# Kernel tuning notes

Measured on AMD Instinct MI355X. Metric: run time of the kernel, lower is better.

Reference implementation:

```python
import jax, jax.numpy as jnp
import numpy as np
from jax import lax

MAX_ITERATIONS = 20


def _min_pool3(x):
    # 3x3x3 min-pool, stride 1, padding 1. Equivalent to -max_pool3d(-x) in
    # torch: padded positions behave as +inf for the min (init value).
    return lax.reduce_window(
        x, jnp.inf, lax.min,
        window_dimensions=(1, 1, 3, 3, 3),
        window_strides=(1, 1, 1, 1, 1),
        padding=[(0, 0), (0, 0), (1, 1), (1, 1), (1, 1)])


def _accumulated_erosion(x, n_iters):
    # dist = sum_{k=1..n} erode^k(x). Torch's early-exit when curr.sum()==0 is
    # a no-op mathematically (erosion of all-zeros stays zero), so a fixed-
    # length scan computes the identical result.
    def body(carry, _):
        curr, dist = carry
        curr = _min_pool3(curr)
        return (curr, dist + curr), None
    (_, dist), _ = lax.scan(body, (x, jnp.zeros_like(x)), None, length=n_iters)
    return dist


def compute_fast_distance_map(target, max_iterations=MAX_ITERATIONS):
    # target: [B, 1, D, H, W] binary float
    dist_in = _accumulated_erosion(target, max_iterations)
    dist_out = _accumulated_erosion(1.0 - target, max_iterations)
    return dist_out * (1.0 - target) - (dist_in - 1.0) * target


def setup_inputs() -> dict:
    key = jax.random.key(0)
    k1, k2 = jax.random.split(key)
    inputs = jax.random.normal(k1, (4, 2, 96, 192, 192), dtype=jnp.float32)
    targets = jax.random.randint(k2, (4, 1, 96, 192, 192), 0, 2, dtype=jnp.int32)
    return {"inputs": inputs, "targets": targets}


def reference(inputs, targets):
    probs = jax.nn.softmax(inputs, axis=1)            # [B, C, D, H, W]
    t = targets.astype(jnp.float32)                   # [B, 1, D, H, W]
    no_fg = jnp.sum(t, axis=(2, 3, 4), keepdims=True) == 0
    dist_map_fg = compute_fast_distance_map(t, MAX_ITERATIONS)
    dist_map_fg = jnp.where(no_fg, jnp.ones_like(dist_map_fg), dist_map_fg)
    probs_fg = probs[:, 1]                            # [B, D, H, W]
    loss = jnp.mean(probs_fg * dist_map_fg[:, 0])
    return loss
```

## Files before the change

kernel.cpp:

```cpp
#include <hip/hip_runtime.h>
#include <hip/hip_bf16.h>

#define BATCH 4
#define DZ 96
#define DY 192
#define DX 192
#define ZS (DY * DX)
#define SVOL ((size_t)DZ * ZS)
#define NTOT ((double)(BATCH * (double)SVOL))
#define VOX_PER_THREAD 8
#define BLOCK 256
#define BLOCKS_PER_BATCH ((int)(SVOL / (VOX_PER_THREAD * BLOCK)))
#define GRID (BATCH * BLOCKS_PER_BATCH)

__device__ __noinline__ int far_dist(const int* __restrict__ T, size_t bOff,
                                     int z, int y, int x, int tv) {
    for (int r = 2; r <= 20; ++r) {
        int zlo = max(z - r, 0), zhi = min(z + r, DZ - 1);
        int ylo = max(y - r, 0), yhi = min(y + r, DY - 1);
        int xlo = max(x - r, 0), xhi = min(x + r, DX - 1);
        for (int zz = zlo; zz <= zhi; ++zz)
            for (int yy = ylo; yy <= yhi; ++yy) {
                const int* rp = T + bOff + (size_t)zz * ZS + (size_t)yy * DX;
                for (int xx = xlo; xx <= xhi; ++xx)
                    if (rp[xx] != tv) return r;
            }
    }
    return 21;
}

__global__ __launch_bounds__(BLOCK) void boundary_loss_kernel(
    const float* __restrict__ inp,
    const int* __restrict__ tgt,
    float4* __restrict__ P)
{
    const int b = blockIdx.x / BLOCKS_PER_BATCH;
    const size_t bOff = (size_t)b * SVOL;
    const int gid = blockIdx.x * BLOCK + threadIdx.x;
    const size_t vox = (size_t)gid * VOX_PER_THREAD;
    const int rem = (int)(vox - bOff);
    const int z = rem / ZS;
    const int ry = rem - z * ZS;
    const int y = ry / DX;
    const int x0 = ry - y * DX;

    uint32_t mxo = ~0u, mxa = 0u;
    if (x0 == 0)      { mxo &= ~1u;        mxa |= 1u; }
    if (x0 == DX - 8) { mxo &= ~(1u << 9); mxa |= (1u << 9); }
    const int ax = (x0 == 0) ? 0 : x0 - 4;
    const int dx8 = (x0 == DX - 8) ? DX - 1 : x0 + 8;

    uint32_t OR9 = 0u, AND9 = ~0u, pc = 0u;
    const int* Tb = tgt + bOff;
    #pragma unroll
    for (int dz = -1; dz <= 1; ++dz) {
        int zz = z + dz;
        if (zz < 0 || zz >= DZ) continue;
        #pragma unroll
        for (int dy = -1; dy <= 1; ++dy) {
            int yy = y + dy;
            if (yy < 0 || yy >= DY) continue;
            const int* rp = Tb + (size_t)zz * ZS + (size_t)yy * DX;
            int4 a = *(const int4*)(rp + ax);
            int4 q = *(const int4*)(rp + x0);
            int4 c = *(const int4*)(rp + x0 + 4);
            int  dd = rp[dx8];
            uint32_t p = (uint32_t)a.w
                | ((uint32_t)q.x << 1) | ((uint32_t)q.y << 2)
                | ((uint32_t)q.z << 3) | ((uint32_t)q.w << 4)
                | ((uint32_t)c.x << 5) | ((uint32_t)c.y << 6)
                | ((uint32_t)c.z << 7) | ((uint32_t)c.w << 8)
                | ((uint32_t)dd  << 9);
            if (dz == 0 && dy == 0) pc = p;
            uint32_t po = p & mxo;
            uint32_t pa = p | mxa;
            OR9  |= po | (po >> 1) | (po >> 2);
            AND9 &= pa & (pa >> 1) & (pa >> 2);
        }
    }
    const uint32_t diff8 = (OR9 ^ AND9) & 0xFFu;
    const uint32_t tc8   = (pc >> 1) & 0xFFu;

    const size_t sp = (size_t)z * ZS + (size_t)y * DX + x0;
    const float* i0 = inp + ((size_t)(2 * b)) * SVOL + sp;
    const float* i1 = i0 + SVOL;
    float4 A0 = *(const float4*)(i0), A1 = *(const float4*)(i0 + 4);
    float4 B0 = *(const float4*)(i1), B1 = *(const float4*)(i1 + 4);
    float c0[8] = {A0.x, A0.y, A0.z, A0.w, A1.x, A1.y, A1.z, A1.w};
    float c1[8] = {B0.x, B0.y, B0.z, B0.w, B1.x, B1.y, B1.z, B1.w};

    float s1 = 0.f, s2 = 0.f;
    #pragma unroll
    for (int i = 0; i < VOX_PER_THREAD; ++i) {
        float e   = __expf(c0[i] - c1[i]);
        float sig = __builtin_amdgcn_rcpf(1.0f + e);
        int ti = (int)((tc8 >> i) & 1u);
        float val = (float)ti;
        if (!((diff8 >> i) & 1u)) {
            int D = far_dist(tgt, bOff, z, y, x0 + i, ti);
            int mm = min(D - 1, 20);
            val = ti ? (1.0f - (float)mm) : (float)mm;
        }
        s1 = fmaf(sig, val, s1);
        s2 += sig;
    }
    float s3 = (tc8 != 0u) ? 1.f : 0.f;

    #pragma unroll
    for (int off = 32; off > 0; off >>= 1) {
        s1 += __shfl_down(s1, off);
        s2 += __shfl_down(s2, off);
        s3 += __shfl_down(s3, off);
    }
    __shared__ float red1[BLOCK / 64], red2[BLOCK / 64], red3[BLOCK / 64];
    const int lane = threadIdx.x & 63, wid = threadIdx.x >> 6;
    if (lane == 0) { red1[wid] = s1; red2[wid] = s2; red3[wid] = s3; }
    __syncthreads();
    if (threadIdx.x == 0) {
        P[blockIdx.x] = make_float4(red1[0] + red1[1] + red1[2] + red1[3],
                                    red2[0] + red2[1] + red2[2] + red2[3],
                                    red3[0] + red3[1] + red3[2] + red3[3], 0.f);
    }
}

__global__ __launch_bounds__(1024) void reduce_kernel(
    const float4* __restrict__ P, float* __restrict__ out)
{
    const int tid = threadIdx.x;
    const int lane = tid & 63, wid = tid >> 6;
    __shared__ double L1[16], L2[16], L3[16];
    double tot = 0.0;

    for (int b = 0; b < BATCH; ++b) {
        double d1 = 0.0, d2 = 0.0, d3 = 0.0;
        for (int i = tid; i < BLOCKS_PER_BATCH; i += 1024) {
            float4 p = P[b * BLOCKS_PER_BATCH + i];
            d1 += p.x; d2 += p.y; d3 += p.z;
        }
        #pragma unroll
        for (int off = 32; off > 0; off >>= 1) {
            d1 += __shfl_down(d1, off);
            d2 += __shfl_down(d2, off);
            d3 += __shfl_down(d3, off);
        }
        if (lane == 0) { L1[wid] = d1; L2[wid] = d2; L3[wid] = d3; }
        __syncthreads();
        if (tid == 0) {
            double s1 = 0.0, s2 = 0.0, s3 = 0.0;
            #pragma unroll
            for (int w = 0; w < 16; ++w) { s1 += L1[w]; s2 += L2[w]; s3 += L3[w]; }
            tot += (s3 > 0.0) ? s1 : s2;
        }
        __syncthreads();
    }
    if (tid == 0) out[0] = (float)(tot / NTOT);
}

extern "C" void kernel_launch(void* const* d_in, const int* in_sizes, int n_in,
                              void* d_out, int out_size, void* d_ws, size_t ws_size,
                              hipStream_t stream) {
    const float* inp = (const float*)d_in[0];
    const int*   tgt = (const int*)d_in[1];
    float* out = (float*)d_out;
    float4* P = (float4*)d_ws;

    hipLaunchKernelGGL(boundary_loss_kernel, dim3(GRID), dim3(BLOCK), 0, stream,
                       inp, tgt, P);
    hipLaunchKernelGGL(reduce_kernel, dim3(1), dim3(1024), 0, stream, P, out);
}
```

Measured before the change: 250.3 us.

## Tile target into LDS bitmask and reuse z-planes across a per-thread column

Each block now covers a 4x16 z-y tile of full x-rows. It packs the target halo into a shared-memory bitmask using atomicOr, and each thread walks 4 z-slices with 12 voxels per slice, reusing the 3x3 neighbourhood plane masks in a rolling window. This replaces the 9 redundant global int4 row loads per thread with LDS bit-window reads, cutting target-read traffic. Costs are LDS atomics, fewer blocks, a larger per-thread register footprint, and clamped halo handling that must still match the border semantics.

```diff
diff --git a/kernel.cpp b/kernel.cpp
--- a/kernel.cpp
+++ b/kernel.cpp
@@ -7,11 +7,20 @@
 #define DX 192
 #define ZS (DY * DX)
 #define SVOL ((size_t)DZ * ZS)
-#define NTOT ((double)(BATCH * (double)SVOL))
-#define VOX_PER_THREAD 8
+#define NTOT ((double)(4.0 * (double)SVOL))
+
+#define ZT 4
+#define YT 16
+#define NZT (DZ / ZT)
+#define NYT (DY / YT)
+#define BLOCKS_PER_BATCH (NZT * NYT)
+#define GRID (BATCH * BLOCKS_PER_BATCH)
 #define BLOCK 256
-#define BLOCKS_PER_BATCH ((int)(SVOL / (VOX_PER_THREAD * BLOCK)))
-#define GRID (BATCH * BLOCKS_PER_BATCH)
+
+#define NP (ZT + 2)
+#define NR (YT + 2)
+#define ROWW 8
+#define LDSW (NP * NR * ROWW)
 
 __device__ __noinline__ int far_dist(const int* __restrict__ T, size_t bOff,
                                      int z, int y, int x, int tv) {
@@ -29,82 +38,110 @@
     return 21;
 }
 
-__global__ __launch_bounds__(BLOCK) void boundary_loss_kernel(
+__global__ __launch_bounds__(BLOCK, 4) void boundary_loss_kernel(
     const float* __restrict__ inp,
     const int* __restrict__ tgt,
     float4* __restrict__ P)
 {
-    const int b = blockIdx.x / BLOCKS_PER_BATCH;
+    const int bi = blockIdx.x;
+    const int b  = bi / BLOCKS_PER_BATCH;
+    const int tr = bi - b * BLOCKS_PER_BATCH;
+    const int zt = tr / NYT;
+    const int yt = tr - zt * NYT;
+    const int z0 = zt * ZT;
+    const int y0 = yt * YT;
     const size_t bOff = (size_t)b * SVOL;
-    const int gid = blockIdx.x * BLOCK + threadIdx.x;
-    const size_t vox = (size_t)gid * VOX_PER_THREAD;
-    const int rem = (int)(vox - bOff);
-    const int z = rem / ZS;
-    const int ry = rem - z * ZS;
-    const int y = ry / DX;
-    const int x0 = ry - y * DX;
-
-    uint32_t mxo = ~0u, mxa = 0u;
-    if (x0 == 0)      { mxo &= ~1u;        mxa |= 1u; }
-    if (x0 == DX - 8) { mxo &= ~(1u << 9); mxa |= (1u << 9); }
-    const int ax = (x0 == 0) ? 0 : x0 - 4;
-    const int dx8 = (x0 == DX - 8) ? DX - 1 : x0 + 8;
-
-    uint32_t OR9 = 0u, AND9 = ~0u, pc = 0u;
     const int* Tb = tgt + bOff;
+
+    __shared__ uint32_t L[LDSW];
+    for (int i = threadIdx.x; i < LDSW; i += BLOCK) L[i] = 0u;
+    __syncthreads();
+    for (int task = threadIdx.x; task < NP * NR * 48; task += BLOCK) {
+        const int rid = task / 48;
+        const int xq  = task - rid * 48;
+        const int pz  = rid / NR;
+        const int py  = rid - pz * NR;
+        const int zz  = min(max(z0 - 1 + pz, 0), DZ - 1);
+        const int yy  = min(max(y0 - 1 + py, 0), DY - 1);
+        const int4 v = *(const int4*)(Tb + (size_t)zz * ZS + (size_t)yy * DX + xq * 4);
+        const uint32_t nib = (uint32_t)(v.x & 1) | ((uint32_t)(v.y & 1) << 1)
+                           | ((uint32_t)(v.z & 1) << 2) | ((uint32_t)(v.w & 1) << 3);
+        atomicOr(&L[rid * ROWW + (xq >> 3)], nib << ((xq & 7) * 4));
+    }
+    __syncthreads();
+
+    const int s  = threadIdx.x & 15;
+    const int r  = threadIdx.x >> 4;
+    const int x0 = s * 12;
+    const int y  = y0 + r;
+
+    const int  q    = (x0 == 0) ? 0 : (x0 - 1);
+    const int  wofs = q >> 5;
+    const int  sh   = q & 31;
+    const bool atL  = (s == 0);
+    const uint32_t forceA = (s == 0 ? 1u : 0u) | (s == 15 ? (1u << 13) : 0u);
+
+    auto rowwin = [&](int pz, int py) -> uint32_t {
+        const uint32_t* Lp = &L[(pz * NR + py) * ROWW + wofs];
+        const uint64_t v = (uint64_t)Lp[0] | ((uint64_t)Lp[1] << 32);
+        return atL ? (uint32_t)((v << 1) & 0x3FFFu)
+                   : (uint32_t)((v >> sh) & 0x3FFFu);
+    };
+
+    uint32_t PO[3], PA[3], TW[3];
+    auto plane = [&](int pz, int slot) {
+        uint32_t o = 0u, a = 0xFFFFFFFFu, tw = 0u;
+        #pragma unroll
+        for (int dy = 0; dy < 3; ++dy) {
+            const uint32_t w  = rowwin(pz, r + dy);
+            if (dy == 1) tw = w;
+            const uint32_t wa = w | forceA;
+            o |= (w | (w >> 1) | (w >> 2));
+            a &= (wa & (wa >> 1) & (wa >> 2));
+        }
+        PO[slot] = o & 0xFFFu; PA[slot] = a & 0xFFFu; TW[slot] = tw;
+    };
+
+    plane(0, 0);
+    plane(1, 1);
+
+    float s1 = 0.f, s2 = 0.f;
+    uint32_t fg = 0u;
+
     #pragma unroll
-    for (int dz = -1; dz <= 1; ++dz) {
-        int zz = z + dz;
-        if (zz < 0 || zz >= DZ) continue;
+    for (int k = 0; k < ZT; ++k) {
+        plane(k + 2, (k + 2) % 3);
+        const int z = z0 + k;
+        const uint32_t diff = (PO[0] | PO[1] | PO[2]) ^ (PA[0] & PA[1] & PA[2]);
+        const uint32_t tc   = (TW[(k + 1) % 3] >> 1) & 0xFFFu;
+        fg |= tc;
+
+        const float* i0 = inp + ((size_t)(2 * b)) * SVOL
+                        + (size_t)z * ZS + (size_t)y * DX + x0;
+        const float* i1 = i0 + SVOL;
+        float4 A0 = *(const float4*)(i0),     A1 = *(const float4*)(i0 + 4),
+               A2 = *(const float4*)(i0 + 8);
+        float4 B0 = *(const float4*)(i1),     B1 = *(const float4*)(i1 + 4),
+               B2 = *(const float4*)(i1 + 8);
+        float c0[12] = {A0.x,A0.y,A0.z,A0.w, A1.x,A1.y,A1.z,A1.w, A2.x,A2.y,A2.z,A2.w};
+        float c1[12] = {B0.x,B0.y,B0.z,B0.w, B1.x,B1.y,B1.z,B1.w, B2.x,B2.y,B2.z,B2.w};
+
         #pragma unroll
-        for (int dy = -1; dy <= 1; ++dy) {
-            int yy = y + dy;
-            if (yy < 0 || yy >= DY) continue;
-            const int* rp = Tb + (size_t)zz * ZS + (size_t)yy * DX;
-            int4 a = *(const int4*)(rp + ax);
-            int4 q = *(const int4*)(rp + x0);
-            int4 c = *(const int4*)(rp + x0 + 4);
-            int  dd = rp[dx8];
-            uint32_t p = (uint32_t)a.w
-                | ((uint32_t)q.x << 1) | ((uint32_t)q.y << 2)
-                | ((uint32_t)q.z << 3) | ((uint32_t)q.w << 4)
-                | ((uint32_t)c.x << 5) | ((uint32_t)c.y << 6)
-                | ((uint32_t)c.z << 7) | ((uint32_t)c.w << 8)
-                | ((uint32_t)dd  << 9);
-            if (dz == 0 && dy == 0) pc = p;
-            uint32_t po = p & mxo;
-            uint32_t pa = p | mxa;
-            OR9  |= po | (po >> 1) | (po >> 2);
-            AND9 &= pa & (pa >> 1) & (pa >> 2);
-        }
-    }
-    const uint32_t diff8 = (OR9 ^ AND9) & 0xFFu;
-    const uint32_t tc8   = (pc >> 1) & 0xFFu;
-
-    const size_t sp = (size_t)z * ZS + (size_t)y * DX + x0;
-    const float* i0 = inp + ((size_t)(2 * b)) * SVOL + sp;
-    const float* i1 = i0 + SVOL;
-    float4 A0 = *(const float4*)(i0), A1 = *(const float4*)(i0 + 4);
-    float4 B0 = *(const float4*)(i1), B1 = *(const float4*)(i1 + 4);
-    float c0[8] = {A0.x, A0.y, A0.z, A0.w, A1.x, A1.y, A1.z, A1.w};
-    float c1[8] = {B0.x, B0.y, B0.z, B0.w, B1.x, B1.y, B1.z, B1.w};
-
-    float s1 = 0.f, s2 = 0.f;
-    #pragma unroll
-    for (int i = 0; i < VOX_PER_THREAD; ++i) {
-        float e   = __expf(c0[i] - c1[i]);
-        float sig = __builtin_amdgcn_rcpf(1.0f + e);
-        int ti = (int)((tc8 >> i) & 1u);
-        float val = (float)ti;
-        if (!((diff8 >> i) & 1u)) {
-            int D = far_dist(tgt, bOff, z, y, x0 + i, ti);
-            int mm = min(D - 1, 20);
-            val = ti ? (1.0f - (float)mm) : (float)mm;
-        }
-        s1 = fmaf(sig, val, s1);
-        s2 += sig;
-    }
-    float s3 = (tc8 != 0u) ? 1.f : 0.f;
+        for (int i = 0; i < 12; ++i) {
+            const float e   = __expf(c0[i] - c1[i]);
+            const float sig = __builtin_amdgcn_rcpf(1.0f + e);
+            const int ti = (int)((tc >> i) & 1u);
+            float val = (float)ti;
+            if (!((diff >> i) & 1u)) {
+                const int D = far_dist(tgt, bOff, z, y, x0 + i, ti);
+                const int mm = min(D - 1, 20);
+                val = ti ? (1.0f - (float)mm) : (float)mm;
+            }
+            s1 = fmaf(sig, val, s1);
+            s2 += sig;
+        }
+    }
+    float s3 = fg ? 1.f : 0.f;
 
     #pragma unroll
     for (int off = 32; off > 0; off >>= 1) {
@@ -146,10 +183,10 @@
         if (lane == 0) { L1[wid] = d1; L2[wid] = d2; L3[wid] = d3; }
         __syncthreads();
         if (tid == 0) {
-            double s1 = 0.0, s2 = 0.0, s3 = 0.0;
+            double t1 = 0.0, t2 = 0.0, t3 = 0.0;
             #pragma unroll
-            for (int w = 0; w < 16; ++w) { s1 += L1[w]; s2 += L2[w]; s3 += L3[w]; }
-            tot += (s3 > 0.0) ? s1 : s2;
+            for (int w = 0; w < 16; ++w) { t1 += L1[w]; t2 += L2[w]; t3 += L3[w]; }
+            tot += (t3 > 0.0) ? t1 : t2;
         }
         __syncthreads();
     }
```

New measurement: 249.5 us. About the same (-0.3%).
